# Performance work log

Hardware: AMD Instinct MI355X
Metric: run time of the kernel (lower is better)

Reference implementation:

```python
import jax, jax.numpy as jnp
import numpy as np

B, C, H, W = 16, 256, 64, 64
OUT_C = 3
N_TOKENS = 512
N_RES = 3
RED = 4
CB = C // RED  # bottleneck channels in ResChain
DN = ('NCHW', 'OIHW', 'NCHW')


def _conv(x, w, pad):
    return jax.lax.conv_general_dilated(x, w, (1, 1), pad, dimension_numbers=DN)


def setup_inputs() -> dict:
    key = jax.random.key(0)
    ks = jax.random.split(key, 8)
    return {
        'input': jax.random.normal(ks[0], (B, C, H, W), jnp.float32),
        'embed': jax.random.normal(ks[1], (C, N_TOKENS), jnp.float32),  # Quantize codebook [dim, n_embed]
        'res_w1': jax.random.normal(ks[2], (N_RES, CB, C, 3, 3), jnp.float32) * 0.02,
        'res_b1': jnp.zeros((N_RES, CB), jnp.float32),
        'res_w2': jax.random.normal(ks[3], (N_RES, C, CB, 1, 1), jnp.float32) * 0.02,
        'res_b2': jnp.zeros((N_RES, C), jnp.float32),
        'out_w': jax.random.normal(ks[4], (OUT_C, C, 1, 1), jnp.float32) * 0.02,
        'out_b': jnp.zeros((OUT_C,), jnp.float32),
    }


def reference(input, embed, res_w1, res_b1, res_w2, res_b2, out_w, out_b):
    sg = jax.lax.stop_gradient
    # --- Quantize (VQ-VAE codebook lookup, straight-through) ---
    x = jnp.transpose(input, (0, 2, 3, 1))  # [B,H,W,C]
    flat = x.reshape(-1, C)                  # [N, C]
    # squared L2 distance to each code: ||f||^2 - 2 f.e + ||e||^2
    dist = (flat * flat).sum(-1, keepdims=True) - 2.0 * (flat @ embed) + (embed * embed).sum(0)
    idx = jnp.argmin(dist, axis=-1).reshape(B, H, W)        # [B,H,W] int
    quantize = jnp.take(embed.T, idx, axis=0)               # embed_code: [B,H,W,C]
    diff = jnp.mean((sg(quantize) - x) ** 2)
    quantize = x + sg(quantize - x)                         # straight-through
    q = jnp.transpose(quantize, (0, 3, 1, 2))               # [B,C,H,W]
    # --- dec: ResChain(n_res_block) + 1x1 conv ---
    for i in range(N_RES):
        h = jax.nn.relu(q)
        h = _conv(h, res_w1[i], 'SAME') + res_b1[i][None, :, None, None]
        h = jax.nn.relu(h)
        h = _conv(h, res_w2[i], 'VALID') + res_b2[i][None, :, None, None]
        q = q + h
    quant = _conv(q, out_w, 'VALID') + out_b[None, :, None, None]  # [B,OUT_C,H,W]
    # --- wordfreq: per-batch bincount over idx (no grad) ---
    flat_idx = idx.reshape(B, -1)
    seg = (flat_idx + jnp.arange(B, dtype=flat_idx.dtype)[:, None] * N_TOKENS).reshape(-1)
    counts = jax.ops.segment_sum(jnp.ones_like(seg, jnp.float32), seg, num_segments=B * N_TOKENS)
    wordfreq = counts.reshape(B, N_TOKENS) / float(H * W)
    return quant, diff.reshape(1), wordfreq
```

## Files before the change

kernel.cpp:

```cpp
#include <hip/hip_runtime.h>


typedef __attribute__((ext_vector_type(8))) short short8;
typedef __attribute__((ext_vector_type(16))) float f32x16;
typedef __attribute__((ext_vector_type(8))) _Float16 half8;
typedef __attribute__((ext_vector_type(2))) _Float16 half2_t;
typedef unsigned short ushort_t;
typedef unsigned long long u64;

#define WS_QA    0
#define WS_QB    8388608
#define WS_ET    16777216
#define WS_EN    16842752
#define WS_EPK   16843264
#define WS_W1PK  16908800
#define WS_W2PK  17129984
#define WS_DIFF  17154560
#define WS_TOK   17154568
#define WS_DST   17220104
#define WS_FN    17285640
#define WS_WL    17351176

#define MARGIN 0.12f

__device__ inline ushort_t f2bf(float f) {
  unsigned u = __float_as_uint(f);
  return (ushort_t)((u + 0x7fffu + ((u >> 16) & 1u)) >> 16);
}
__device__ inline float bf2f(ushort_t h) { return __uint_as_float(((unsigned)h) << 16); }
union HU { _Float16 h; ushort_t u; };
union S8H { short8 s; half8 h; half2_t h2[4]; };

__global__ __launch_bounds__(256) void prep_kernel(
    const float* __restrict__ embed, const float* __restrict__ w1,
    const float* __restrict__ w2, float* __restrict__ ws, float* __restrict__ wf) {
  int i = blockIdx.x * 256 + threadIdx.x;
  if (i < 131072) {
    int t = i >> 8, c = i & 255;
    ((ushort_t*)(ws + WS_ET))[i] = f2bf(embed[c * 512 + t]);
  }
  if (i < 512) {
    float s = 0.f;
    for (int c = 0; c < 256; ++c) { float v = embed[c * 512 + i]; s += v * v; }
    ws[WS_EN + i] = s;
  }
  if (i < 131072) {
    int j = i & 7, lane = (i >> 3) & 63, at = (i >> 9) & 15, ks = i >> 13;
    int code = at * 32 + (lane & 31);
    int c = ks * 16 + (lane >> 5) * 8 + j;
    HU cv; cv.h = (_Float16)embed[c * 512 + code];
    ((ushort_t*)(ws + WS_EPK))[i] = cv.u;
  }
  if (i < 442368) {
    int j = i & 7; int lane = (i >> 3) & 63; int of = (i >> 9) & 1;
    int k16 = (i >> 10) & 15; int rest = i >> 14;
    int tap = rest % 9; int layer = rest / 9;
    int oc = of * 32 + (lane & 31);
    int c = k16 * 16 + (lane >> 5) * 8 + j;
    ((ushort_t*)(ws + WS_W1PK))[i] = f2bf(w1[((layer * 64 + oc) * 256 + c) * 9 + tap]);
  }
  if (i < 49152) {
    int j = i & 7, lane = (i >> 3) & 63, at = (i >> 9) & 7, ks = (i >> 12) & 3, l = i >> 14;
    int co = at * 32 + (lane & 31), cb = ks * 16 + (lane >> 5) * 8 + j;
    ((ushort_t*)(ws + WS_W2PK))[i] = f2bf(w2[(l * 256 + co) * 64 + cb]);
  }
  if (i < 8192) wf[i] = 0.f;
  if (i == 0) { ws[WS_DIFF] = 0.f; ((int*)(ws + WS_WL))[0] = 0; }
}

__global__ __launch_bounds__(512, 4) void dist_kernel(
    const float* __restrict__ input, const half8* __restrict__ epk,
    const float* __restrict__ enorm, int* __restrict__ tok,
    float* __restrict__ dst, float* __restrict__ fnv, int* __restrict__ wl) {
  __shared__ __align__(16) ushort_t sfp[2048 * 8];
  __shared__ float senorm[512];
  __shared__ float trim1[512], trim2[512];
  __shared__ int   trii[512];

  int blk = blockIdx.x, b = blk >> 6, hw0 = (blk & 63) << 6;
  int tid = threadIdx.x, lane = tid & 63, wave = tid >> 6;
  senorm[tid] = enorm[tid];

  {
    int cg = tid >> 3, sub = tid & 7;
    int ks_s = cg >> 2, hi_s = (cg >> 1) & 1, jq = cg & 1;
    const float* src0 = input + ((size_t)(b * 256 + cg * 4)) * 4096 + hw0 + sub * 8;
    float vv[4][8];
#pragma unroll
    for (int m = 0; m < 4; ++m) {
      const float4* s4 = (const float4*)(src0 + (size_t)m * 4096);
      float4 aa = s4[0], bb = s4[1];
      vv[m][0] = aa.x; vv[m][1] = aa.y; vv[m][2] = aa.z; vv[m][3] = aa.w;
      vv[m][4] = bb.x; vv[m][5] = bb.y; vv[m][6] = bb.z; vv[m][7] = bb.w;
    }
    u64* sfp64 = (u64*)sfp;
#pragma unroll
    for (int i = 0; i < 8; ++i) {
      int pl = sub * 8 + i;
      int bt = pl >> 5, lw = (pl & 31) + 32 * hi_s;
      u64 pk = 0;
#pragma unroll
      for (int m = 0; m < 4; ++m) {
        HU cv; cv.h = (_Float16)vv[m][i];
        pk |= ((u64)cv.u) << (16 * m);
      }
      sfp64[((bt * 16 + ks_s) * 64 + lw) * 2 + jq] = pk;
    }
  }
  __syncthreads();

  f32x16 acc[2][2];
#pragma unroll
  for (int bt = 0; bt < 2; ++bt)
#pragma unroll
    for (int a = 0; a < 2; ++a)
#pragma unroll
      for (int r = 0; r < 16; ++r) acc[bt][a][r] = 0.f;

  const short8* sfp8 = (const short8*)sfp;
  float fnp0 = 0.f, fnp1 = 0.f;
#pragma unroll 2
  for (int ks = 0; ks < 16; ++ks) {
    S8H u0, u1;
    u0.s = sfp8[ks * 64 + lane];
    u1.s = sfp8[(16 + ks) * 64 + lane];
#if __has_builtin(__builtin_amdgcn_fdot2)
#pragma unroll
    for (int k = 0; k < 4; ++k) {
      fnp0 = __builtin_amdgcn_fdot2(u0.h2[k], u0.h2[k], fnp0, false);
      fnp1 = __builtin_amdgcn_fdot2(u1.h2[k], u1.h2[k], fnp1, false);
    }
#else
#pragma unroll
    for (int k = 0; k < 8; ++k) {
      float v0 = (float)u0.h[k], v1 = (float)u1.h[k];
      fnp0 += v0 * v0; fnp1 += v1 * v1;
    }
#endif
#pragma unroll
    for (int a = 0; a < 2; ++a) {
      half8 ah = epk[(ks * 16 + wave * 2 + a) * 64 + lane];
      acc[0][a] = __builtin_amdgcn_mfma_f32_32x32x16_f16(ah, u0.h, acc[0][a], 0, 0, 0);
      acc[1][a] = __builtin_amdgcn_mfma_f32_32x32x16_f16(ah, u1.h, acc[1][a], 0, 0, 0);
    }
  }
  fnp0 += __shfl_xor(fnp0, 32, 64);
  fnp1 += __shfl_xor(fnp1, 32, 64);

  int hi5 = lane >> 5;
#pragma unroll
  for (int bt = 0; bt < 2; ++bt) {
    float m1 = 3.4e38f, m2 = 3.4e38f; int i1 = 0;
#pragma unroll
    for (int a = 0; a < 2; ++a)
#pragma unroll
      for (int r = 0; r < 16; ++r) {
        int code = (wave * 2 + a) * 32 + (r & 3) + 8 * (r >> 2) + 4 * hi5;
        float v = senorm[code] - 2.0f * acc[bt][a][r];
        if (v < m1) { m2 = m1; m1 = v; i1 = code; }
        else if (v < m2) m2 = v;
      }
    float o1 = __shfl_xor(m1, 32, 64);
    float o2 = __shfl_xor(m2, 32, 64);
    int   oi = __shfl_xor(i1, 32, 64);
    float n2 = fminf(fmaxf(m1, o1), fminf(m2, o2));
    float n1 = fminf(m1, o1);
    int   ni = (o1 < m1) ? oi : i1;
    if (lane < 32) {
      int p = bt * 32 + lane;
      trim1[p * 8 + wave] = n1; trim2[p * 8 + wave] = n2; trii[p * 8 + wave] = ni;
    }
  }
  __syncthreads();

  if (wave == 0) {
    int p = lane;
    float m1 = trim1[p * 8], m2 = trim2[p * 8]; int i1 = trii[p * 8];
#pragma unroll
    for (int w = 1; w < 8; ++w) {
      float a1 = trim1[p * 8 + w], a2 = trim2[p * 8 + w]; int ai = trii[p * 8 + w];
      float n2 = fminf(fmaxf(m1, a1), fminf(m2, a2));
      if (a1 < m1) { m1 = a1; i1 = ai; }
      m2 = n2;
    }
    float myfn = (lane < 32) ? fnp0 : fnp1;
    int gpos = blk * 64 + p;
    tok[gpos] = i1;
    dst[gpos] = myfn + m1;
    fnv[gpos] = myfn;
    bool flag = (m2 - m1 < MARGIN);
    u64 mk = __ballot(flag);
    int base = 0;
    if (lane == 0 && mk) base = atomicAdd(wl, (int)__popcll(mk));
    base = __shfl(base, 0, 64);
    if (flag) {
      int off = (int)__popcll(mk & ((1ull << lane) - 1ull));
      wl[1 + base + off] = gpos;
    }
  }
}

__global__ __launch_bounds__(256) void redo_kernel(
    const float* __restrict__ input, const float* __restrict__ embed,
    const float* __restrict__ enorm, const int* __restrict__ wl,
    int* __restrict__ tok, float* __restrict__ dst, const float* __restrict__ fnv) {
  __shared__ float sf[256], rv[256];
  __shared__ int   ri[256];
  int n = wl[0];
  int tid = threadIdx.x;
  for (int e = blockIdx.x; e < n; e += gridDim.x) {
    int gpos = wl[1 + e];
    int b = gpos >> 12, hw = gpos & 4095;
    sf[tid] = input[((size_t)(b * 256 + tid)) * 4096 + hw];
    __syncthreads();
    float d0 = 0.f, d1 = 0.f;
#pragma unroll 4
    for (int c = 0; c < 256; ++c) {
      float fv = sf[c];
      d0 += fv * embed[c * 512 + tid];
      d1 += fv * embed[c * 512 + 256 + tid];
    }
    float v0 = enorm[tid] - 2.f * d0;
    float v1 = enorm[256 + tid] - 2.f * d1;
    float bv; int bi;
    if (v1 < v0) { bv = v1; bi = 256 + tid; } else { bv = v0; bi = tid; }
    rv[tid] = bv; ri[tid] = bi;
    __syncthreads();
    for (int s = 128; s > 0; s >>= 1) {
      if (tid < s) {
        float ov = rv[tid + s]; int oi2 = ri[tid + s];
        if (ov < rv[tid] || (ov == rv[tid] && oi2 < ri[tid])) { rv[tid] = ov; ri[tid] = oi2; }
      }
      __syncthreads();
    }
    if (tid == 0) { tok[gpos] = ri[0]; dst[gpos] = fnv[gpos] + rv[0]; }
    __syncthreads();
  }
}

__global__ __launch_bounds__(256) void finalize_kernel(
    const int* __restrict__ tok, const float* __restrict__ dst,
    const ushort_t* __restrict__ embedT, float* __restrict__ wf,
    float* __restrict__ diffp, ushort_t* __restrict__ qout) {
  int blk = blockIdx.x;
  int tid = threadIdx.x, lane = tid & 63, wave = tid >> 6;
  int gbase = blk * 64;
  int b = gbase >> 12;
  if (wave == 0) {
    int t = tok[gbase + lane];
    atomicAdd(&wf[b * 512 + t], 1.0f / 4096.0f);
    float d = dst[gbase + lane];
#pragma unroll
    for (int off = 32; off >= 1; off >>= 1) d += __shfl_down(d, off, 64);
    if (lane == 0) atomicAdd(diffp, d);
  }
#pragma unroll 1
  for (int j = 0; j < 16; ++j) {
    int p = wave * 16 + j;
    int t = __builtin_amdgcn_readfirstlane(tok[gbase + p]);
    const u64* src = (const u64*)(embedT + (size_t)t * 256);
    u64* dstp = (u64*)(qout + ((size_t)(gbase + p)) * 256);
    dstp[lane] = src[lane];
  }
}

__global__ __launch_bounds__(256, 4) void fused_layer(
    const ushort_t* __restrict__ qin, ushort_t* __restrict__ qout,
    const ushort_t* __restrict__ w1pk, const float* __restrict__ b1,
    const ushort_t* __restrict__ w2pk, const float* __restrict__ b2, int l) {
  __shared__ __align__(16) char arena[38912];
  ushort_t* hbuf   = (ushort_t*)arena;
  float*    sb2    = (float*)(arena + 9728);
  short8*   stg    = (short8*)(arena + 10752);
  ushort_t* qstage = (ushort_t*)(arena + 10752);

  int blk = blockIdx.x;
  int b = blk >> 6; int t = blk & 63;
  int ty0 = (t >> 3) << 3;
  int tx0 = (t & 7) << 3;
  int tid = threadIdx.x, lane = tid & 63, w = tid >> 6;
  int pt = w & 1, ot = w >> 1;
  int l31 = lane & 31, kb5 = lane >> 5;

  sb2[tid] = b2[l * 256 + tid];

  const short8* wp  = (const short8*)w1pk + (size_t)l * 18432;
  const short8* w2p = (const short8*)w2pk;

  short8 sreg[4];
  auto loadch = [&](int cs) {
#pragma unroll
    for (int s = 0; s < 4; ++s) {
      int u = s * 256 + tid;
      if (u < 800) {
        int cg = u & 7; int pix = u >> 3; int y = pix / 10; int x = pix - y * 10;
        int sy = ty0 + y - 1, sx = tx0 + x - 1;
        if (sy >= 0 && sy < 64 && sx >= 0 && sx < 64) {
          sreg[s] = *(const short8*)(qin + ((size_t)(b * 4096 + sy * 64 + sx)) * 256 + cs * 64 + cg * 8);
        } else {
          short8 z;
#pragma unroll
          for (int k2 = 0; k2 < 8; ++k2) z[k2] = 0;
          sreg[s] = z;
        }
      }
    }
  };
  auto writech = [&](int buf) {
#pragma unroll
    for (int s = 0; s < 4; ++s) {
      int u = s * 256 + tid;
      if (u < 800) {
        int cg = u & 7; int pix = u >> 3; int y = pix / 10; int x = pix - y * 10;
        short8 sv = sreg[s];
#pragma unroll
        for (int k2 = 0; k2 < 8; ++k2) if (sv[k2] < 0) sv[k2] = 0;
        stg[buf * 880 + (y * 8 + cg) * 11 + x] = sv;
      }
    }
  };

  f32x16 acc;
#pragma unroll
  for (int r = 0; r < 16; ++r) acc[r] = 0.f;

  int py0 = pt * 4 + (l31 >> 3);
  int px0 = lane & 7;

  loadch(0);
  writech(0);
#pragma unroll 1
  for (int cs = 0; cs < 4; ++cs) {
    __syncthreads();
    if (cs < 3) loadch(cs + 1);
    int buf = cs & 1;
#pragma unroll 1
    for (int dy = 0; dy < 3; ++dy) {
#pragma unroll 1
      for (int dx = 0; dx < 3; ++dx) {
        int tap = dy * 3 + dx;
#pragma unroll
        for (int ks2 = 0; ks2 < 4; ++ks2) {
          short8 A = stg[buf * 880 + ((py0 + dy) * 8 + ks2 * 2 + kb5) * 11 + px0 + dx];
          short8 B = wp[(tap * 16 + cs * 4 + ks2) * 128 + ot * 64 + lane];
          acc = __builtin_amdgcn_mfma_f32_32x32x16_bf16(A, B, acc, 0, 0, 0);
        }
      }
    }
    if (cs < 3) writech((cs + 1) & 1);
  }
  __syncthreads();

  {
    int oc = ot * 32 + l31;
    float bb = b1[l * 64 + oc];
#pragma unroll
    for (int r = 0; r < 16; ++r) {
      int row = (r & 3) + 8 * (r >> 2) + 4 * kb5;
      hbuf[(pt * 32 + row) * 76 + oc] = f2bf(fmaxf(acc[r] + bb, 0.f));
    }
  }
  __syncthreads();

  int pt2 = w & 1, coq = w >> 1;
#pragma unroll 1
  for (int ch = 0; ch < 2; ++ch) {
    short8 qv[4];
#pragma unroll
    for (int it = 0; it < 4; ++it) {
      int u = it * 256 + tid;
      int p = u >> 4, c8 = u & 15;
      int gy = ty0 + (p >> 3), gx = tx0 + (p & 7);
      qv[it] = *(const short8*)(qin + ((size_t)(b * 4096 + gy * 64 + gx)) * 256 + ch * 128 + c8 * 8);
    }

    f32x16 acc2[2];
#pragma unroll
    for (int a = 0; a < 2; ++a)
#pragma unroll
      for (int r = 0; r < 16; ++r) acc2[a][r] = 0.f;

#pragma unroll
    for (int ks = 0; ks < 4; ++ks) {
      short8 A = *(const short8*)(hbuf + (pt2 * 32 + l31) * 76 + ks * 16 + kb5 * 8);
#pragma unroll
      for (int a = 0; a < 2; ++a) {
        short8 B = w2p[((l * 4 + ks) * 8 + ch * 4 + coq * 2 + a) * 64 + lane];
        acc2[a] = __builtin_amdgcn_mfma_f32_32x32x16_bf16(A, B, acc2[a], 0, 0, 0);
      }
    }
#pragma unroll
    for (int a = 0; a < 2; ++a) {
      int cc = coq * 64 + a * 32 + l31;
      float bb2 = sb2[ch * 128 + cc];
#pragma unroll
      for (int r = 0; r < 16; ++r) {
        int row = (r & 3) + 8 * (r >> 2) + 4 * kb5;
        qstage[(pt2 * 32 + row) * 136 + cc] = f2bf(acc2[a][r] + bb2);
      }
    }
    __syncthreads();
#pragma unroll
    for (int it = 0; it < 4; ++it) {
      int u = it * 256 + tid;
      int p = u >> 4, c8 = u & 15;
      short8 hv = *(const short8*)(qstage + p * 136 + c8 * 8);
      int gy = ty0 + (p >> 3), gx = tx0 + (p & 7);
      size_t gidx = ((size_t)(b * 4096 + gy * 64 + gx)) * 256 + ch * 128 + c8 * 8;
      short8 ov;
#pragma unroll
      for (int k2 = 0; k2 < 8; ++k2)
        ov[k2] = (short)f2bf(bf2f((ushort_t)qv[it][k2]) + bf2f((ushort_t)hv[k2]));
      *(short8*)(qout + gidx) = ov;
    }
    __syncthreads();
  }
}

__global__ __launch_bounds__(256) void final_kernel(
    const ushort_t* __restrict__ qbuf, const float* __restrict__ ow,
    const float* __restrict__ ob, float* __restrict__ out,
    const float* __restrict__ ws) {
  int t = blockIdx.x * 256 + threadIdx.x;
  int pos = t >> 4, c16 = t & 15;
  const ushort_t* qp = qbuf + (size_t)pos * 256 + c16 * 16;
  short8 v0 = *(const short8*)qp;
  short8 v1 = *(const short8*)(qp + 8);
  float a0 = 0.f, a1 = 0.f, a2 = 0.f;
#pragma unroll
  for (int k = 0; k < 16; ++k) {
    float f = bf2f((ushort_t)(k < 8 ? v0[k] : v1[k - 8]));
    int c = c16 * 16 + k;
    a0 += f * ow[c];
    a1 += f * ow[256 + c];
    a2 += f * ow[512 + c];
  }
#pragma unroll
  for (int off = 1; off < 16; off <<= 1) {
    a0 += __shfl_xor(a0, off, 64);
    a1 += __shfl_xor(a1, off, 64);
    a2 += __shfl_xor(a2, off, 64);
  }
  if (c16 == 0) {
    int b = pos >> 12, hw = pos & 4095;
    out[(b * 3 + 0) * 4096 + hw] = a0 + ob[0];
    out[(b * 3 + 1) * 4096 + hw] = a1 + ob[1];
    out[(b * 3 + 2) * 4096 + hw] = a2 + ob[2];
  }
  if (t == 0) out[196608] = ws[WS_DIFF] * (1.0f / 16777216.0f);
}

extern "C" void kernel_launch(void* const* d_in, const int* in_sizes, int n_in,
                              void* d_out, int out_size, void* d_ws, size_t ws_size,
                              hipStream_t stream) {
  (void)in_sizes; (void)n_in; (void)out_size; (void)ws_size;
  const float* input = (const float*)d_in[0];
  const float* embed = (const float*)d_in[1];
  const float* b1 = (const float*)d_in[3];
  const float* b2 = (const float*)d_in[5];
  const float* ow = (const float*)d_in[6];
  const float* ob = (const float*)d_in[7];
  float* ws = (float*)d_ws;
  float* out = (float*)d_out;
  float* wf = out + 196609;

  ushort_t* qA = (ushort_t*)(ws + WS_QA);
  ushort_t* qB = (ushort_t*)(ws + WS_QB);
  const ushort_t* et = (const ushort_t*)(ws + WS_ET);
  const half8* epk = (const half8*)(ws + WS_EPK);
  const ushort_t* w1pk = (const ushort_t*)(ws + WS_W1PK);
  const ushort_t* w2pk = (const ushort_t*)(ws + WS_W2PK);
  int*   tok = (int*)(ws + WS_TOK);
  float* dst = ws + WS_DST;
  float* fnv = ws + WS_FN;
  int*   wl  = (int*)(ws + WS_WL);

  hipLaunchKernelGGL(prep_kernel, dim3(1728), dim3(256), 0, stream,
                     embed, (const float*)d_in[2], (const float*)d_in[4], ws, wf);
  hipLaunchKernelGGL(dist_kernel, dim3(1024), dim3(512), 0, stream,
                     input, epk, ws + WS_EN, tok, dst, fnv, wl);
  hipLaunchKernelGGL(redo_kernel, dim3(1024), dim3(256), 0, stream,
                     input, embed, ws + WS_EN, wl, tok, dst, fnv);
  hipLaunchKernelGGL(finalize_kernel, dim3(1024), dim3(256), 0, stream,
                     tok, dst, et, wf, ws + WS_DIFF, qA);
  hipLaunchKernelGGL(fused_layer, dim3(1024), dim3(256), 0, stream,
                     qA, qB, w1pk, b1, w2pk, b2, 0);
  hipLaunchKernelGGL(fused_layer, dim3(1024), dim3(256), 0, stream,
                     qB, qA, w1pk, b1, w2pk, b2, 1);
  hipLaunchKernelGGL(fused_layer, dim3(1024), dim3(256), 0, stream,
                     qA, qB, w1pk, b1, w2pk, b2, 2);
  hipLaunchKernelGGL(final_kernel, dim3(4096), dim3(256), 0, stream,
                     qB, ow, ob, out, ws);
}
```

Baseline: 239.4 us.

## Double fused_layer block to 512 threads with split-K 3x3 conv and LDS reduction

Raises the fused residual layer from 256 to 512 threads per block. The 3x3 conv's K dimension (channel sub-slices) is split across two wave groups, whose partial accumulators are reduced through shared memory before bias and ReLU. The 1x1 conv's output channels are also spread over 8 waves, and staging loads are redistributed. The aim is more waves per block to hide latency, at the cost of an extra LDS reduction pass, an extra barrier and higher register pressure under launch_bounds(512,4).

```diff
diff --git a/kernel.cpp b/kernel.cpp
--- a/kernel.cpp
+++ b/kernel.cpp
@@ -264,7 +264,7 @@
   }
 }
 
-__global__ __launch_bounds__(256, 4) void fused_layer(
+__global__ __launch_bounds__(512, 4) void fused_layer(
     const ushort_t* __restrict__ qin, ushort_t* __restrict__ qout,
     const ushort_t* __restrict__ w1pk, const float* __restrict__ b1,
     const ushort_t* __restrict__ w2pk, const float* __restrict__ b2, int l) {
@@ -272,6 +272,7 @@
   ushort_t* hbuf   = (ushort_t*)arena;
   float*    sb2    = (float*)(arena + 9728);
   short8*   stg    = (short8*)(arena + 10752);
+  float*    red    = (float*)(arena + 10752);
   ushort_t* qstage = (ushort_t*)(arena + 10752);
 
   int blk = blockIdx.x;
@@ -279,19 +280,19 @@
   int ty0 = (t >> 3) << 3;
   int tx0 = (t & 7) << 3;
   int tid = threadIdx.x, lane = tid & 63, w = tid >> 6;
-  int pt = w & 1, ot = w >> 1;
+  int pt = w & 1, ot = (w >> 1) & 1, kh = w >> 2;
   int l31 = lane & 31, kb5 = lane >> 5;
 
-  sb2[tid] = b2[l * 256 + tid];
+  if (tid < 256) sb2[tid] = b2[l * 256 + tid];
 
   const short8* wp  = (const short8*)w1pk + (size_t)l * 18432;
   const short8* w2p = (const short8*)w2pk;
 
-  short8 sreg[4];
+  short8 sreg[2];
   auto loadch = [&](int cs) {
 #pragma unroll
-    for (int s = 0; s < 4; ++s) {
-      int u = s * 256 + tid;
+    for (int s = 0; s < 2; ++s) {
+      int u = s * 512 + tid;
       if (u < 800) {
         int cg = u & 7; int pix = u >> 3; int y = pix / 10; int x = pix - y * 10;
         int sy = ty0 + y - 1, sx = tx0 + x - 1;
@@ -308,8 +309,8 @@
   };
   auto writech = [&](int buf) {
 #pragma unroll
-    for (int s = 0; s < 4; ++s) {
-      int u = s * 256 + tid;
+    for (int s = 0; s < 2; ++s) {
+      int u = s * 512 + tid;
       if (u < 800) {
         int cg = u & 7; int pix = u >> 3; int y = pix / 10; int x = pix - y * 10;
         short8 sv = sreg[s];
@@ -340,9 +341,10 @@
       for (int dx = 0; dx < 3; ++dx) {
         int tap = dy * 3 + dx;
 #pragma unroll
-        for (int ks2 = 0; ks2 < 4; ++ks2) {
-          short8 A = stg[buf * 880 + ((py0 + dy) * 8 + ks2 * 2 + kb5) * 11 + px0 + dx];
-          short8 B = wp[(tap * 16 + cs * 4 + ks2) * 128 + ot * 64 + lane];
+        for (int ks2 = 0; ks2 < 2; ++ks2) {
+          int kk = kh * 2 + ks2;
+          short8 A = stg[buf * 880 + ((py0 + dy) * 8 + kk * 2 + kb5) * 11 + px0 + dx];
+          short8 B = wp[(tap * 16 + cs * 4 + kk) * 128 + ot * 64 + lane];
           acc = __builtin_amdgcn_mfma_f32_32x32x16_bf16(A, B, acc, 0, 0, 0);
         }
       }
@@ -351,13 +353,24 @@
   }
   __syncthreads();
 
-  {
+  if (kh == 1) {
+    float4* d = (float4*)(red + (w & 3) * 1024 + lane * 16);
+#pragma unroll
+    for (int r4 = 0; r4 < 4; ++r4) {
+      float4 v; v.x = acc[r4 * 4]; v.y = acc[r4 * 4 + 1];
+      v.z = acc[r4 * 4 + 2]; v.w = acc[r4 * 4 + 3];
+      d[r4] = v;
+    }
+  }
+  __syncthreads();
+  if (kh == 0) {
+    const float* s = red + (w & 3) * 1024 + lane * 16;
     int oc = ot * 32 + l31;
     float bb = b1[l * 64 + oc];
 #pragma unroll
     for (int r = 0; r < 16; ++r) {
       int row = (r & 3) + 8 * (r >> 2) + 4 * kb5;
-      hbuf[(pt * 32 + row) * 76 + oc] = f2bf(fmaxf(acc[r] + bb, 0.f));
+      hbuf[(pt * 32 + row) * 76 + oc] = f2bf(fmaxf(acc[r] + s[r] + bb, 0.f));
     }
   }
   __syncthreads();
@@ -365,44 +378,37 @@
   int pt2 = w & 1, coq = w >> 1;
 #pragma unroll 1
   for (int ch = 0; ch < 2; ++ch) {
-    short8 qv[4];
-#pragma unroll
-    for (int it = 0; it < 4; ++it) {
-      int u = it * 256 + tid;
+    short8 qv[2];
+#pragma unroll
+    for (int it = 0; it < 2; ++it) {
+      int u = it * 512 + tid;
       int p = u >> 4, c8 = u & 15;
       int gy = ty0 + (p >> 3), gx = tx0 + (p & 7);
       qv[it] = *(const short8*)(qin + ((size_t)(b * 4096 + gy * 64 + gx)) * 256 + ch * 128 + c8 * 8);
     }
 
-    f32x16 acc2[2];
-#pragma unroll
-    for (int a = 0; a < 2; ++a)
-#pragma unroll
-      for (int r = 0; r < 16; ++r) acc2[a][r] = 0.f;
-
+    f32x16 acc2;
+#pragma unroll
+    for (int r = 0; r < 16; ++r) acc2[r] = 0.f;
 #pragma unroll
     for (int ks = 0; ks < 4; ++ks) {
       short8 A = *(const short8*)(hbuf + (pt2 * 32 + l31) * 76 + ks * 16 + kb5 * 8);
-#pragma unroll
-      for (int a = 0; a < 2; ++a) {
-        short8 B = w2p[((l * 4 + ks) * 8 + ch * 4 + coq * 2 + a) * 64 + lane];
-        acc2[a] = __builtin_amdgcn_mfma_f32_32x32x16_bf16(A, B, acc2[a], 0, 0, 0);
-      }
-    }
-#pragma unroll
-    for (int a = 0; a < 2; ++a) {
-      int cc = coq * 64 + a * 32 + l31;
+      short8 B = w2p[((l * 4 + ks) * 8 + ch * 4 + coq) * 64 + lane];
+      acc2 = __builtin_amdgcn_mfma_f32_32x32x16_bf16(A, B, acc2, 0, 0, 0);
+    }
+    {
+      int cc = coq * 32 + l31;
       float bb2 = sb2[ch * 128 + cc];
 #pragma unroll
       for (int r = 0; r < 16; ++r) {
         int row = (r & 3) + 8 * (r >> 2) + 4 * kb5;
-        qstage[(pt2 * 32 + row) * 136 + cc] = f2bf(acc2[a][r] + bb2);
+        qstage[(pt2 * 32 + row) * 136 + cc] = f2bf(acc2[r] + bb2);
       }
     }
     __syncthreads();
 #pragma unroll
-    for (int it = 0; it < 4; ++it) {
-      int u = it * 256 + tid;
+    for (int it = 0; it < 2; ++it) {
+      int u = it * 512 + tid;
       int p = u >> 4, c8 = u & 15;
       short8 hv = *(const short8*)(qstage + p * 136 + c8 * 8);
       int gy = ty0 + (p >> 3), gx = tx0 + (p & 7);
@@ -483,11 +489,11 @@
                      input, embed, ws + WS_EN, wl, tok, dst, fnv);
   hipLaunchKernelGGL(finalize_kernel, dim3(1024), dim3(256), 0, stream,
                      tok, dst, et, wf, ws + WS_DIFF, qA);
-  hipLaunchKernelGGL(fused_layer, dim3(1024), dim3(256), 0, stream,
+  hipLaunchKernelGGL(fused_layer, dim3(1024), dim3(512), 0, stream,
                      qA, qB, w1pk, b1, w2pk, b2, 0);
-  hipLaunchKernelGGL(fused_layer, dim3(1024), dim3(256), 0, stream,
+  hipLaunchKernelGGL(fused_layer, dim3(1024), dim3(512), 0, stream,
                      qB, qA, w1pk, b1, w2pk, b2, 1);
-  hipLaunchKernelGGL(fused_layer, dim3(1024), dim3(256), 0, stream,
+  hipLaunchKernelGGL(fused_layer, dim3(1024), dim3(512), 0, stream,
                      qA, qB, w1pk, b1, w2pk, b2, 2);
   hipLaunchKernelGGL(final_kernel, dim3(4096), dim3(256), 0, stream,
                      qB, ow, ob, out, ws);
```

Result: faster. 229.8 us (-4.0%).

## Enlarge fused residual layer tile to 8x16 pixels and single-buffer halo staging

Applied to the files above, without the earlier changes.

Each fused_layer block now covers an 8x16 pixel tile instead of 8x8, so grid size halves to 512 blocks. Each wave computes two 32-row MFMA tiles per weight fragment, so every B (weight) load from global is reused twice and the halo overhead per pixel drops. The staging buffer moves from double to single buffering with an extra barrier per channel slice. The 1x1 conv epilogue is restructured into four 64-channel chunks. The costs are fewer blocks (512 on a large GPU, possibly underfilling CUs), a lower occupancy hint (3), more registers, and less overlap of loads with MFMA.

```diff
diff --git a/kernel.cpp b/kernel.cpp
--- a/kernel.cpp
+++ b/kernel.cpp
@@ -264,22 +264,22 @@
   }
 }
 
-__global__ __launch_bounds__(256, 4) void fused_layer(
+__global__ __launch_bounds__(256, 3) void fused_layer(
     const ushort_t* __restrict__ qin, ushort_t* __restrict__ qout,
     const ushort_t* __restrict__ w1pk, const float* __restrict__ b1,
     const ushort_t* __restrict__ w2pk, const float* __restrict__ b2, int l) {
-  __shared__ __align__(16) char arena[38912];
-  ushort_t* hbuf   = (ushort_t*)arena;
-  float*    sb2    = (float*)(arena + 9728);
-  short8*   stg    = (short8*)(arena + 10752);
-  ushort_t* qstage = (ushort_t*)(arena + 10752);
+  __shared__ __align__(16) char arena[42496];
+  short8*   stg    = (short8*)arena;
+  ushort_t* qstage = (ushort_t*)arena;
+  ushort_t* hbuf   = (ushort_t*)(arena + 23040);
+  float*    sb2    = (float*)(arena + 41472);
 
   int blk = blockIdx.x;
-  int b = blk >> 6; int t = blk & 63;
-  int ty0 = (t >> 3) << 3;
-  int tx0 = (t & 7) << 3;
+  int b = blk >> 5; int t = blk & 31;
+  int ty0 = (t >> 2) << 3;
+  int tx0 = (t & 3) << 4;
   int tid = threadIdx.x, lane = tid & 63, w = tid >> 6;
-  int pt = w & 1, ot = w >> 1;
+  int pt = w >> 1, ot = w & 1;
   int l31 = lane & 31, kb5 = lane >> 5;
 
   sb2[tid] = b2[l * 256 + tid];
@@ -287,14 +287,14 @@
   const short8* wp  = (const short8*)w1pk + (size_t)l * 18432;
   const short8* w2p = (const short8*)w2pk;
 
-  short8 sreg[4];
+  short8 sreg[6];
   auto loadch = [&](int cs) {
 #pragma unroll
-    for (int s = 0; s < 4; ++s) {
+    for (int s = 0; s < 6; ++s) {
       int u = s * 256 + tid;
-      if (u < 800) {
-        int cg = u & 7; int pix = u >> 3; int y = pix / 10; int x = pix - y * 10;
-        int sy = ty0 + y - 1, sx = tx0 + x - 1;
+      if (u < 1440) {
+        int xx = u % 18; int r = u / 18; int cg = r & 7; int yy = r >> 3;
+        int sy = ty0 + yy - 1, sx = tx0 + xx - 1;
         if (sy >= 0 && sy < 64 && sx >= 0 && sx < 64) {
           sreg[s] = *(const short8*)(qin + ((size_t)(b * 4096 + sy * 64 + sx)) * 256 + cs * 64 + cg * 8);
         } else {
@@ -306,107 +306,115 @@
       }
     }
   };
-  auto writech = [&](int buf) {
-#pragma unroll
-    for (int s = 0; s < 4; ++s) {
+  auto writech = [&]() {
+#pragma unroll
+    for (int s = 0; s < 6; ++s) {
       int u = s * 256 + tid;
-      if (u < 800) {
-        int cg = u & 7; int pix = u >> 3; int y = pix / 10; int x = pix - y * 10;
+      if (u < 1440) {
         short8 sv = sreg[s];
 #pragma unroll
         for (int k2 = 0; k2 < 8; ++k2) if (sv[k2] < 0) sv[k2] = 0;
-        stg[buf * 880 + (y * 8 + cg) * 11 + x] = sv;
+        stg[u] = sv;
       }
     }
   };
 
-  f32x16 acc;
-#pragma unroll
-  for (int r = 0; r < 16; ++r) acc[r] = 0.f;
-
-  int py0 = pt * 4 + (l31 >> 3);
-  int px0 = lane & 7;
+  f32x16 acc[2];
+#pragma unroll
+  for (int mi = 0; mi < 2; ++mi)
+#pragma unroll
+    for (int r = 0; r < 16; ++r) acc[mi][r] = 0.f;
+
+  int y0 = pt * 4 + (l31 >> 4);
+  int x0 = l31 & 15;
 
   loadch(0);
-  writech(0);
+  writech();
+  __syncthreads();
 #pragma unroll 1
   for (int cs = 0; cs < 4; ++cs) {
-    __syncthreads();
     if (cs < 3) loadch(cs + 1);
-    int buf = cs & 1;
 #pragma unroll 1
     for (int dy = 0; dy < 3; ++dy) {
 #pragma unroll 1
       for (int dx = 0; dx < 3; ++dx) {
         int tap = dy * 3 + dx;
 #pragma unroll
-        for (int ks2 = 0; ks2 < 4; ++ks2) {
-          short8 A = stg[buf * 880 + ((py0 + dy) * 8 + ks2 * 2 + kb5) * 11 + px0 + dx];
-          short8 B = wp[(tap * 16 + cs * 4 + ks2) * 128 + ot * 64 + lane];
-          acc = __builtin_amdgcn_mfma_f32_32x32x16_bf16(A, B, acc, 0, 0, 0);
+        for (int kk = 0; kk < 4; ++kk) {
+          int base = ((y0 + dy) * 8 + kk * 2 + kb5) * 18 + (x0 + dx);
+          short8 A0 = stg[base];
+          short8 A1 = stg[base + 288];
+          short8 B = wp[(tap * 16 + cs * 4 + kk) * 128 + ot * 64 + lane];
+          acc[0] = __builtin_amdgcn_mfma_f32_32x32x16_bf16(A0, B, acc[0], 0, 0, 0);
+          acc[1] = __builtin_amdgcn_mfma_f32_32x32x16_bf16(A1, B, acc[1], 0, 0, 0);
         }
       }
     }
-    if (cs < 3) writech((cs + 1) & 1);
-  }
-  __syncthreads();
+    __syncthreads();
+    if (cs < 3) { writech(); __syncthreads(); }
+  }
 
   {
     int oc = ot * 32 + l31;
     float bb = b1[l * 64 + oc];
 #pragma unroll
-    for (int r = 0; r < 16; ++r) {
-      int row = (r & 3) + 8 * (r >> 2) + 4 * kb5;
-      hbuf[(pt * 32 + row) * 76 + oc] = f2bf(fmaxf(acc[r] + bb, 0.f));
-    }
+    for (int mi = 0; mi < 2; ++mi)
+#pragma unroll
+      for (int r = 0; r < 16; ++r) {
+        int row = (r & 3) + 8 * (r >> 2) + 4 * kb5;
+        int px = (2 * pt + mi) * 32 + row;
+        hbuf[px * 72 + oc] = f2bf(fmaxf(acc[mi][r] + bb, 0.f));
+      }
   }
   __syncthreads();
 
-  int pt2 = w & 1, coq = w >> 1;
+  int pt2 = w >> 1, coh = w & 1;
 #pragma unroll 1
-  for (int ch = 0; ch < 2; ++ch) {
+  for (int cq = 0; cq < 4; ++cq) {
     short8 qv[4];
 #pragma unroll
     for (int it = 0; it < 4; ++it) {
       int u = it * 256 + tid;
-      int p = u >> 4, c8 = u & 15;
-      int gy = ty0 + (p >> 3), gx = tx0 + (p & 7);
-      qv[it] = *(const short8*)(qin + ((size_t)(b * 4096 + gy * 64 + gx)) * 256 + ch * 128 + c8 * 8);
-    }
-
-    f32x16 acc2[2];
-#pragma unroll
-    for (int a = 0; a < 2; ++a)
-#pragma unroll
-      for (int r = 0; r < 16; ++r) acc2[a][r] = 0.f;
+      int px = u >> 3, c8 = u & 7;
+      int gy = ty0 + (px >> 4), gx = tx0 + (px & 15);
+      qv[it] = *(const short8*)(qin + ((size_t)(b * 4096 + gy * 64 + gx)) * 256 + cq * 64 + c8 * 8);
+    }
+
+    f32x16 a2[2];
+#pragma unroll
+    for (int mi = 0; mi < 2; ++mi)
+#pragma unroll
+      for (int r = 0; r < 16; ++r) a2[mi][r] = 0.f;
 
 #pragma unroll
     for (int ks = 0; ks < 4; ++ks) {
-      short8 A = *(const short8*)(hbuf + (pt2 * 32 + l31) * 76 + ks * 16 + kb5 * 8);
-#pragma unroll
-      for (int a = 0; a < 2; ++a) {
-        short8 B = w2p[((l * 4 + ks) * 8 + ch * 4 + coq * 2 + a) * 64 + lane];
-        acc2[a] = __builtin_amdgcn_mfma_f32_32x32x16_bf16(A, B, acc2[a], 0, 0, 0);
-      }
-    }
-#pragma unroll
-    for (int a = 0; a < 2; ++a) {
-      int cc = coq * 64 + a * 32 + l31;
-      float bb2 = sb2[ch * 128 + cc];
-#pragma unroll
-      for (int r = 0; r < 16; ++r) {
-        int row = (r & 3) + 8 * (r >> 2) + 4 * kb5;
-        qstage[(pt2 * 32 + row) * 136 + cc] = f2bf(acc2[a][r] + bb2);
-      }
+      short8 Bw = w2p[((l * 4 + ks) * 8 + cq * 2 + coh) * 64 + lane];
+#pragma unroll
+      for (int mi = 0; mi < 2; ++mi) {
+        short8 A = *(const short8*)(hbuf + ((2 * pt2 + mi) * 32 + l31) * 72 + ks * 16 + kb5 * 8);
+        a2[mi] = __builtin_amdgcn_mfma_f32_32x32x16_bf16(A, Bw, a2[mi], 0, 0, 0);
+      }
+    }
+    {
+      int cc = coh * 32 + l31;
+      float bb2 = sb2[cq * 64 + cc];
+#pragma unroll
+      for (int mi = 0; mi < 2; ++mi)
+#pragma unroll
+        for (int r = 0; r < 16; ++r) {
+          int row = (r & 3) + 8 * (r >> 2) + 4 * kb5;
+          int px = (2 * pt2 + mi) * 32 + row;
+          qstage[px * 72 + cc] = f2bf(a2[mi][r] + bb2);
+        }
     }
     __syncthreads();
 #pragma unroll
     for (int it = 0; it < 4; ++it) {
       int u = it * 256 + tid;
-      int p = u >> 4, c8 = u & 15;
-      short8 hv = *(const short8*)(qstage + p * 136 + c8 * 8);
-      int gy = ty0 + (p >> 3), gx = tx0 + (p & 7);
-      size_t gidx = ((size_t)(b * 4096 + gy * 64 + gx)) * 256 + ch * 128 + c8 * 8;
+      int px = u >> 3, c8 = u & 7;
+      short8 hv = *(const short8*)(qstage + px * 72 + c8 * 8);
+      int gy = ty0 + (px >> 4), gx = tx0 + (px & 15);
+      size_t gidx = ((size_t)(b * 4096 + gy * 64 + gx)) * 256 + cq * 64 + c8 * 8;
       short8 ov;
 #pragma unroll
       for (int k2 = 0; k2 < 8; ++k2)
@@ -483,11 +491,11 @@
                      input, embed, ws + WS_EN, wl, tok, dst, fnv);
   hipLaunchKernelGGL(finalize_kernel, dim3(1024), dim3(256), 0, stream,
                      tok, dst, et, wf, ws + WS_DIFF, qA);
-  hipLaunchKernelGGL(fused_layer, dim3(1024), dim3(256), 0, stream,
+  hipLaunchKernelGGL(fused_layer, dim3(512), dim3(256), 0, stream,
                      qA, qB, w1pk, b1, w2pk, b2, 0);
-  hipLaunchKernelGGL(fused_layer, dim3(1024), dim3(256), 0, stream,
+  hipLaunchKernelGGL(fused_layer, dim3(512), dim3(256), 0, stream,
                      qB, qA, w1pk, b1, w2pk, b2, 1);
-  hipLaunchKernelGGL(fused_layer, dim3(1024), dim3(256), 0, stream,
+  hipLaunchKernelGGL(fused_layer, dim3(512), dim3(256), 0, stream,
                      qA, qB, w1pk, b1, w2pk, b2, 2);
   hipLaunchKernelGGL(final_kernel, dim3(4096), dim3(256), 0, stream,
                      qB, ow, ob, out, ws);
```

Result: no change. 236.0 us (-1.4%).
